# Kernel tuning notes

Measured on AMD Instinct MI355X. Metric: run time of the kernel, lower is better.

The kernel has to match this reference:

```python
import jax, jax.numpy as jnp
import numpy as np

K = 7            # involution kernel size
GC = 16          # group_channels (hardcoded in module)
EPS = 1e-5       # BatchNorm eps


def setup_inputs() -> dict:
    key = jax.random.key(0)
    ks = jax.random.split(key, 5)
    C, R = 256, 4
    mid = C // R                      # 64
    groups = C // GC                  # 16
    B, H, W = 4, 56, 56
    x = jax.random.normal(ks[0], (B, C, H, W), dtype=jnp.float32)
    w1 = jax.random.normal(ks[1], (mid, C), dtype=jnp.float32) * (1.0 / np.sqrt(C))
    b1 = jax.random.normal(ks[2], (mid,), dtype=jnp.float32) * 0.01
    gamma = jnp.ones((mid,), dtype=jnp.float32)
    beta = jnp.zeros((mid,), dtype=jnp.float32)
    w2 = jax.random.normal(ks[3], (K * K * groups, mid), dtype=jnp.float32) * (1.0 / np.sqrt(mid))
    b2 = jax.random.normal(ks[4], (K * K * groups,), dtype=jnp.float32) * 0.01
    return {"x": x, "w1": w1, "b1": b1, "gamma": gamma, "beta": beta, "w2": w2, "b2": b2}


def reference(x, w1, b1, gamma, beta, w2, b2):
    B, C, H, W = x.shape
    groups = C // GC
    k2 = K * K
    pad = (K - 1) // 2

    # weight branch: 1x1 conv -> BN (batch stats, training-mode math) -> ReLU -> 1x1 conv
    t = jnp.einsum('oc,bchw->bohw', w1, x) + b1[None, :, None, None]
    mu = t.mean(axis=(0, 2, 3), keepdims=True)
    var = ((t - mu) ** 2).mean(axis=(0, 2, 3), keepdims=True)
    t = (t - mu) * jax.lax.rsqrt(var + EPS)
    t = t * gamma[None, :, None, None] + beta[None, :, None, None]
    t = jax.nn.relu(t)
    wgt = jnp.einsum('ot,bthw->bohw', w2, t) + b2[None, :, None, None]
    wgt = wgt.reshape(B, groups, k2, H, W)              # per-pixel kernels

    # unfold: kernel positions row-major (i over kh, j over kw), channel-major layout
    xp = jnp.pad(x, ((0, 0), (0, 0), (pad, pad), (pad, pad)))
    patches = jnp.stack(
        [xp[:, :, i:i + H, j:j + W] for i in range(K) for j in range(K)], axis=2
    )                                                   # [B, C, k2, H, W]
    patches = patches.reshape(B, groups, GC, k2, H, W)

    out = jnp.einsum('bgkhw,bgckhw->bgchw', wgt, patches)  # weighted sum over k2
    return out.reshape(B, C, H, W)
```

## Files before the change

### kernel.cpp

```cpp
#include <hip/hip_runtime.h>

#define KSZ   7
#define KK    49
#define GCH   16
#define CIN   256
#define MID   64
#define NGRP  16
#define WID   56
#define HWSZ  3136
#define NB    4
#define NPIX  (NB * HWSZ)
#define EPSV  1e-5f


__global__ __launch_bounds__(256) void k1_conv1(const float* __restrict__ x,
                                                const float* __restrict__ w1,
                                                const float* __restrict__ b1,
                                                float* __restrict__ ws) {
    const int tid = threadIdx.x;
    const int pix = blockIdx.x * 256 + tid;
    const int ob  = blockIdx.y * 16;
    const int b   = pix / HWSZ;
    const int hw  = pix - b * HWSZ;

    float acc[16];
#pragma unroll
    for (int i = 0; i < 16; ++i) acc[i] = b1[ob + i];

    const float* xp = x + (size_t)b * CIN * HWSZ + hw;
#pragma unroll 4
    for (int c = 0; c < CIN; ++c) {
        const float xv = xp[(size_t)c * HWSZ];
#pragma unroll
        for (int i = 0; i < 16; ++i)
            acc[i] = fmaf(w1[(ob + i) * CIN + c], xv, acc[i]);
    }

    float* tp = ws + 256 + (size_t)b * MID * HWSZ + (size_t)ob * HWSZ + hw;
#pragma unroll
    for (int i = 0; i < 16; ++i) tp[(size_t)i * HWSZ] = acc[i];

    __shared__ float bs[16];
    __shared__ float bq[16];
    if (tid < 16) { bs[tid] = 0.f; bq[tid] = 0.f; }
    __syncthreads();

#pragma unroll
    for (int i = 0; i < 16; ++i) {
        float s = acc[i];
        float q = acc[i] * acc[i];
#pragma unroll
        for (int m = 1; m < 64; m <<= 1) {
            s += __shfl_xor(s, m, 64);
            q += __shfl_xor(q, m, 64);
        }
        if ((tid & 63) == 0) {
            atomicAdd(&bs[i], s);
            atomicAdd(&bq[i], q);
        }
    }
    __syncthreads();
    if (tid < 16) {
        atomicAdd(&ws[ob + tid],      bs[tid]);
        atomicAdd(&ws[64 + ob + tid], bq[tid]);
    }
}

__global__ void k2_stats(float* __restrict__ ws,
                         const float* __restrict__ gamma,
                         const float* __restrict__ beta) {
    const int o = threadIdx.x;
    const float n   = (float)NPIX;
    const float mu  = ws[o] / n;
    const float var = ws[64 + o] / n - mu * mu;
    const float a   = gamma[o] * rsqrtf(var + EPSV);
    ws[128 + o] = a;
    ws[192 + o] = beta[o] - mu * a;
}

__global__ __launch_bounds__(256) void k3_fused(const float* __restrict__ x,
                                                const float* __restrict__ w2,
                                                const float* __restrict__ b2,
                                                const float* __restrict__ ws,
                                                float* __restrict__ out) {
    const int tid = threadIdx.x;
    const int pix = blockIdx.x * 256 + tid;
    const int g   = blockIdx.y;
    const int b   = pix / HWSZ;
    const int hw  = pix - b * HWSZ;
    const int h   = hw / WID;
    const int w   = hw - h * WID;

    const float* tp = ws + 256 + (size_t)b * MID * HWSZ + hw;
    float tn[MID];
#pragma unroll
    for (int o = 0; o < MID; ++o) {
        const float v = tp[(size_t)o * HWSZ];
        tn[o] = fmaxf(0.f, fmaf(ws[128 + o], v, ws[192 + o]));
    }

    float acc[GCH];
#pragma unroll
    for (int cc = 0; cc < GCH; ++cc) acc[cc] = 0.f;

    const float* xg = x + ((size_t)b * CIN + (size_t)g * GCH) * HWSZ;

    for (int k = 0; k < KK; ++k) {
        const int j = g * KK + k;
        const float* wr = w2 + (size_t)j * MID;
        float d0 = 0.f, d1 = 0.f, d2 = 0.f, d3 = 0.f;
#pragma unroll
        for (int o = 0; o < MID; o += 4) {
            d0 = fmaf(wr[o    ], tn[o    ], d0);
            d1 = fmaf(wr[o + 1], tn[o + 1], d1);
            d2 = fmaf(wr[o + 2], tn[o + 2], d2);
            d3 = fmaf(wr[o + 3], tn[o + 3], d3);
        }
        const float wgt = b2[j] + ((d0 + d1) + (d2 + d3));

        const int kd = k / 7;
        const int di = kd - 3;
        const int dj = (k - kd * 7) - 3;
        const int hh = h + di;
        const int wwv = w + dj;
        const bool valid = ((unsigned)hh < 56u) && ((unsigned)wwv < 56u);
        const float wm = valid ? wgt : 0.f;
        const int hhc = valid ? hh : 0;
        const int wwc = valid ? wwv : 0;
        const float* xb = xg + hhc * WID + wwc;
#pragma unroll
        for (int cc = 0; cc < GCH; ++cc)
            acc[cc] = fmaf(wm, xb[(size_t)cc * HWSZ], acc[cc]);
    }

    float* ob = out + ((size_t)b * CIN + (size_t)g * GCH) * HWSZ + hw;
#pragma unroll
    for (int cc = 0; cc < GCH; ++cc) ob[(size_t)cc * HWSZ] = acc[cc];
}

extern "C" void kernel_launch(void* const* d_in, const int* in_sizes, int n_in,
                              void* d_out, int out_size, void* d_ws, size_t ws_size,
                              hipStream_t stream) {
    const float* x     = (const float*)d_in[0];
    const float* w1    = (const float*)d_in[1];
    const float* b1    = (const float*)d_in[2];
    const float* gamma = (const float*)d_in[3];
    const float* beta  = (const float*)d_in[4];
    const float* w2    = (const float*)d_in[5];
    const float* b2    = (const float*)d_in[6];
    float* out = (float*)d_out;
    float* ws  = (float*)d_ws;

    hipMemsetAsync(ws, 0, 128 * sizeof(float), stream);

    k1_conv1<<<dim3(49, 4), 256, 0, stream>>>(x, w1, b1, ws);
    k2_stats<<<1, 64, 0, stream>>>(ws, gamma, beta);
    k3_fused<<<dim3(49, 16), 256, 0, stream>>>(x, w2, b2, ws, out);
}
```

Before: 113.6 us.

## Shrink blocks to single wavefronts, store intermediate pixel-major, restructure weight generation

Both main kernels now use 64-thread blocks, and conv1 handles 8 output channels per block, giving many more blocks. The intermediate activation is stored pixel-major so each pixel's 64 values are written and read as float4 vectors. The fused kernel accumulates all 49 per-pixel kernel weights while streaming the mid channels, instead of keeping 64 normalized values live and recomputing dot products per tap. Stats reduction drops the shared-memory stage and each wave issues global atomics directly, which raises atomic traffic. Holding 49 accumulators may also raise register pressure.

```diff
diff --git a/kernel.cpp b/kernel.cpp
--- a/kernel.cpp
+++ b/kernel.cpp
@@ -13,40 +13,35 @@
 #define EPSV  1e-5f
 
 
-__global__ __launch_bounds__(256) void k1_conv1(const float* __restrict__ x,
-                                                const float* __restrict__ w1,
-                                                const float* __restrict__ b1,
-                                                float* __restrict__ ws) {
+__global__ __launch_bounds__(64, 4) void k1_conv1(const float* __restrict__ x,
+                                                  const float* __restrict__ w1,
+                                                  const float* __restrict__ b1,
+                                                  float* __restrict__ ws) {
     const int tid = threadIdx.x;
-    const int pix = blockIdx.x * 256 + tid;
-    const int ob  = blockIdx.y * 16;
+    const int pix = blockIdx.x * 64 + tid;
+    const int ob  = blockIdx.y * 8;
     const int b   = pix / HWSZ;
     const int hw  = pix - b * HWSZ;
 
-    float acc[16];
+    float acc[8];
 #pragma unroll
-    for (int i = 0; i < 16; ++i) acc[i] = b1[ob + i];
+    for (int i = 0; i < 8; ++i) acc[i] = b1[ob + i];
 
     const float* xp = x + (size_t)b * CIN * HWSZ + hw;
-#pragma unroll 4
+#pragma unroll 8
     for (int c = 0; c < CIN; ++c) {
         const float xv = xp[(size_t)c * HWSZ];
 #pragma unroll
-        for (int i = 0; i < 16; ++i)
+        for (int i = 0; i < 8; ++i)
             acc[i] = fmaf(w1[(ob + i) * CIN + c], xv, acc[i]);
     }
 
-    float* tp = ws + 256 + (size_t)b * MID * HWSZ + (size_t)ob * HWSZ + hw;
-#pragma unroll
-    for (int i = 0; i < 16; ++i) tp[(size_t)i * HWSZ] = acc[i];
-
-    __shared__ float bs[16];
-    __shared__ float bq[16];
-    if (tid < 16) { bs[tid] = 0.f; bq[tid] = 0.f; }
-    __syncthreads();
+    float4* tp = (float4*)(ws + 256 + (size_t)pix * MID + ob);
+    tp[0] = make_float4(acc[0], acc[1], acc[2], acc[3]);
+    tp[1] = make_float4(acc[4], acc[5], acc[6], acc[7]);
 
 #pragma unroll
-    for (int i = 0; i < 16; ++i) {
+    for (int i = 0; i < 8; ++i) {
         float s = acc[i];
         float q = acc[i] * acc[i];
 #pragma unroll
@@ -54,15 +49,10 @@
             s += __shfl_xor(s, m, 64);
             q += __shfl_xor(q, m, 64);
         }
-        if ((tid & 63) == 0) {
-            atomicAdd(&bs[i], s);
-            atomicAdd(&bq[i], q);
+        if (tid == 0) {
+            atomicAdd(&ws[ob + i],      s);
+            atomicAdd(&ws[64 + ob + i], q);
         }
-    }
-    __syncthreads();
-    if (tid < 16) {
-        atomicAdd(&ws[ob + tid],      bs[tid]);
-        atomicAdd(&ws[64 + ob + tid], bq[tid]);
     }
 }
 
@@ -78,25 +68,44 @@
     ws[192 + o] = beta[o] - mu * a;
 }
 
-__global__ __launch_bounds__(256) void k3_fused(const float* __restrict__ x,
-                                                const float* __restrict__ w2,
-                                                const float* __restrict__ b2,
-                                                const float* __restrict__ ws,
-                                                float* __restrict__ out) {
+__global__ __launch_bounds__(64, 4) void k3_fused(const float* __restrict__ x,
+                                                  const float* __restrict__ w2,
+                                                  const float* __restrict__ b2,
+                                                  const float* __restrict__ ws,
+                                                  float* __restrict__ out) {
     const int tid = threadIdx.x;
-    const int pix = blockIdx.x * 256 + tid;
+    const int pix = blockIdx.x * 64 + tid;
     const int g   = blockIdx.y;
     const int b   = pix / HWSZ;
     const int hw  = pix - b * HWSZ;
     const int h   = hw / WID;
     const int w   = hw - h * WID;
 
-    const float* tp = ws + 256 + (size_t)b * MID * HWSZ + hw;
-    float tn[MID];
+    float wgt[KK];
+    const float* w2g = w2 + (size_t)g * KK * MID;
+    const float* b2g = b2 + (size_t)g * KK;
 #pragma unroll
-    for (int o = 0; o < MID; ++o) {
-        const float v = tp[(size_t)o * HWSZ];
-        tn[o] = fmaxf(0.f, fmaf(ws[128 + o], v, ws[192 + o]));
+    for (int k = 0; k < KK; ++k) wgt[k] = b2g[k];
+
+    const float* tb = ws + 256 + (size_t)pix * MID;
+    for (int oc = 0; oc < MID; oc += 8) {
+        const float4 v0 = *(const float4*)(tb + oc);
+        const float4 v1 = *(const float4*)(tb + oc + 4);
+        float tv[8];
+        tv[0] = fmaxf(0.f, fmaf(ws[128 + oc + 0], v0.x, ws[192 + oc + 0]));
+        tv[1] = fmaxf(0.f, fmaf(ws[128 + oc + 1], v0.y, ws[192 + oc + 1]));
+        tv[2] = fmaxf(0.f, fmaf(ws[128 + oc + 2], v0.z, ws[192 + oc + 2]));
+        tv[3] = fmaxf(0.f, fmaf(ws[128 + oc + 3], v0.w, ws[192 + oc + 3]));
+        tv[4] = fmaxf(0.f, fmaf(ws[128 + oc + 4], v1.x, ws[192 + oc + 4]));
+        tv[5] = fmaxf(0.f, fmaf(ws[128 + oc + 5], v1.y, ws[192 + oc + 5]));
+        tv[6] = fmaxf(0.f, fmaf(ws[128 + oc + 6], v1.z, ws[192 + oc + 6]));
+        tv[7] = fmaxf(0.f, fmaf(ws[128 + oc + 7], v1.w, ws[192 + oc + 7]));
+#pragma unroll
+        for (int k = 0; k < KK; ++k) {
+#pragma unroll
+            for (int o = 0; o < 8; ++o)
+                wgt[k] = fmaf(w2g[k * MID + oc + o], tv[o], wgt[k]);
+        }
     }
 
     float acc[GCH];
@@ -105,29 +114,15 @@
 
     const float* xg = x + ((size_t)b * CIN + (size_t)g * GCH) * HWSZ;
 
+#pragma unroll
     for (int k = 0; k < KK; ++k) {
-        const int j = g * KK + k;
-        const float* wr = w2 + (size_t)j * MID;
-        float d0 = 0.f, d1 = 0.f, d2 = 0.f, d3 = 0.f;
-#pragma unroll
-        for (int o = 0; o < MID; o += 4) {
-            d0 = fmaf(wr[o    ], tn[o    ], d0);
-            d1 = fmaf(wr[o + 1], tn[o + 1], d1);
-            d2 = fmaf(wr[o + 2], tn[o + 2], d2);
-            d3 = fmaf(wr[o + 3], tn[o + 3], d3);
-        }
-        const float wgt = b2[j] + ((d0 + d1) + (d2 + d3));
-
-        const int kd = k / 7;
-        const int di = kd - 3;
-        const int dj = (k - kd * 7) - 3;
-        const int hh = h + di;
+        const int di = k / 7 - 3;
+        const int dj = k % 7 - 3;
+        const int hh  = h + di;
         const int wwv = w + dj;
         const bool valid = ((unsigned)hh < 56u) && ((unsigned)wwv < 56u);
-        const float wm = valid ? wgt : 0.f;
-        const int hhc = valid ? hh : 0;
-        const int wwc = valid ? wwv : 0;
-        const float* xb = xg + hhc * WID + wwc;
+        const float wm = valid ? wgt[k] : 0.f;
+        const float* xb = xg + (valid ? hh * WID + wwv : 0);
 #pragma unroll
         for (int cc = 0; cc < GCH; ++cc)
             acc[cc] = fmaf(wm, xb[(size_t)cc * HWSZ], acc[cc]);
@@ -153,7 +148,7 @@
 
     hipMemsetAsync(ws, 0, 128 * sizeof(float), stream);
 
-    k1_conv1<<<dim3(49, 4), 256, 0, stream>>>(x, w1, b1, ws);
+    k1_conv1<<<dim3(196, 8), 64, 0, stream>>>(x, w1, b1, ws);
     k2_stats<<<1, 64, 0, stream>>>(ws, gamma, beta);
-    k3_fused<<<dim3(49, 16), 256, 0, stream>>>(x, w2, b2, ws, out);
+    k3_fused<<<dim3(196, 16), 64, 0, stream>>>(x, w2, b2, ws, out);
 }
```

Result: slower. 285.1 us (+151.0%).

## Stage normalized activations in LDS and compute kernel weights by row

Applied to the files above, without the earlier changes.

The intermediate activations are now stored pixel-major across the whole batch (o*NPIX + pix), so a block can straddle batch boundaries. In k3 the 64 normalized activations per pixel go into shared memory instead of a 64-entry register array, which should cut register pressure and raise occupancy. Kernel weights are now computed seven at a time, one kernel row per pass, which interleaves the w2 dot products with the unfold accumulation. The cost is 64 KB of LDS per block and a barrier, and that LDS size may itself limit how many blocks fit on a CU.

```diff
diff --git a/kernel.cpp b/kernel.cpp
--- a/kernel.cpp
+++ b/kernel.cpp
@@ -36,9 +36,9 @@
             acc[i] = fmaf(w1[(ob + i) * CIN + c], xv, acc[i]);
     }
 
-    float* tp = ws + 256 + (size_t)b * MID * HWSZ + (size_t)ob * HWSZ + hw;
+    float* tp = ws + 256 + (size_t)ob * NPIX + pix;
 #pragma unroll
-    for (int i = 0; i < 16; ++i) tp[(size_t)i * HWSZ] = acc[i];
+    for (int i = 0; i < 16; ++i) tp[(size_t)i * NPIX] = acc[i];
 
     __shared__ float bs[16];
     __shared__ float bq[16];
@@ -83,6 +83,7 @@
                                                 const float* __restrict__ b2,
                                                 const float* __restrict__ ws,
                                                 float* __restrict__ out) {
+    __shared__ float tl[MID][256];
     const int tid = threadIdx.x;
     const int pix = blockIdx.x * 256 + tid;
     const int g   = blockIdx.y;
@@ -91,49 +92,51 @@
     const int h   = hw / WID;
     const int w   = hw - h * WID;
 
-    const float* tp = ws + 256 + (size_t)b * MID * HWSZ + hw;
-    float tn[MID];
-#pragma unroll
+    const float* tcol = ws + 256 + pix;
+#pragma unroll 8
     for (int o = 0; o < MID; ++o) {
-        const float v = tp[(size_t)o * HWSZ];
-        tn[o] = fmaxf(0.f, fmaf(ws[128 + o], v, ws[192 + o]));
+        const float v = tcol[(size_t)o * NPIX];
+        tl[o][tid] = fmaxf(0.f, fmaf(ws[128 + o], v, ws[192 + o]));
     }
+    __syncthreads();
 
     float acc[GCH];
 #pragma unroll
     for (int cc = 0; cc < GCH; ++cc) acc[cc] = 0.f;
 
-    const float* xg = x + ((size_t)b * CIN + (size_t)g * GCH) * HWSZ;
+    const float* w2g = w2 + (size_t)g * KK * MID;
+    const float* b2g = b2 + (size_t)g * KK;
+    const int   xbase = (b * CIN + g * GCH) * HWSZ;
 
-    for (int k = 0; k < KK; ++k) {
-        const int j = g * KK + k;
-        const float* wr = w2 + (size_t)j * MID;
-        float d0 = 0.f, d1 = 0.f, d2 = 0.f, d3 = 0.f;
+    for (int kc = 0; kc < 7; ++kc) {
+        float aw[7];
 #pragma unroll
-        for (int o = 0; o < MID; o += 4) {
-            d0 = fmaf(wr[o    ], tn[o    ], d0);
-            d1 = fmaf(wr[o + 1], tn[o + 1], d1);
-            d2 = fmaf(wr[o + 2], tn[o + 2], d2);
-            d3 = fmaf(wr[o + 3], tn[o + 3], d3);
+        for (int j = 0; j < 7; ++j) aw[j] = b2g[kc * 7 + j];
+
+#pragma unroll 8
+        for (int o = 0; o < MID; ++o) {
+            const float tv = tl[o][tid];
+#pragma unroll
+            for (int j = 0; j < 7; ++j)
+                aw[j] = fmaf(w2g[(kc * 7 + j) * MID + o], tv, aw[j]);
         }
-        const float wgt = b2[j] + ((d0 + d1) + (d2 + d3));
 
-        const int kd = k / 7;
-        const int di = kd - 3;
-        const int dj = (k - kd * 7) - 3;
-        const int hh = h + di;
-        const int wwv = w + dj;
-        const bool valid = ((unsigned)hh < 56u) && ((unsigned)wwv < 56u);
-        const float wm = valid ? wgt : 0.f;
-        const int hhc = valid ? hh : 0;
-        const int wwc = valid ? wwv : 0;
-        const float* xb = xg + hhc * WID + wwc;
+        const int  hh    = h + kc - 3;
+        const bool rowok = (unsigned)hh < 56u;
 #pragma unroll
-        for (int cc = 0; cc < GCH; ++cc)
-            acc[cc] = fmaf(wm, xb[(size_t)cc * HWSZ], acc[cc]);
+        for (int j = 0; j < 7; ++j) {
+            const int  ww = w + j - 3;
+            const bool ok = rowok && ((unsigned)ww < 56u);
+            const float wm = ok ? aw[j] : 0.f;
+            const int  off = ok ? (hh * WID + ww) : 0;
+            const float* xb = x + xbase + off;
+#pragma unroll
+            for (int cc = 0; cc < GCH; ++cc)
+                acc[cc] = fmaf(wm, xb[(size_t)cc * HWSZ], acc[cc]);
+        }
     }
 
-    float* ob = out + ((size_t)b * CIN + (size_t)g * GCH) * HWSZ + hw;
+    float* ob = out + (size_t)xbase + hw;
 #pragma unroll
     for (int cc = 0; cc < GCH; ++cc) ob[(size_t)cc * HWSZ] = acc[cc];
 }
```

Result: slower. 148.1 us (+30.4%).
